# Performance work log

Hardware: AMD Instinct MI355X
Metric: run time of the kernel (lower is better)

The kernel has to match this reference:

```python
import jax, jax.numpy as jnp
import numpy as np

N_CLUSTERS = 64
N_GHOST = 2
EPS = 1e-12  # F.normalize eps


def setup_inputs() -> dict:
    key = jax.random.key(0)
    k1, k2, k3, k4 = jax.random.split(key, 4)
    n_utts, feat_dim, duration = 16, 256, 1500
    x = jax.random.normal(k1, (n_utts, feat_dim, duration), dtype=jnp.float32)
    centroids = jax.random.uniform(k2, (N_CLUSTERS, feat_dim), dtype=jnp.float32)
    # NetVLAD init ties linear.weight = 2*alpha*centroids(+ghosts); here independent params suffice for a math baseline
    lin_w = jax.random.normal(k3, (N_CLUSTERS + N_GHOST, feat_dim), dtype=jnp.float32)
    lin_b = jax.random.normal(k4, (N_CLUSTERS + N_GHOST,), dtype=jnp.float32)
    return {"x": x, "centroids": centroids, "lin_w": lin_w, "lin_b": lin_b}


def reference(x, centroids, lin_w, lin_b):
    # x: [u, f, t] -> [u, t, f]
    n_utts = x.shape[0]
    xt = jnp.transpose(x, (0, 2, 1))
    # soft assignments over clusters+ghosts, then drop ghost columns
    logits = jnp.einsum('utf,cf->utc', xt, lin_w) + lin_b  # [u,t,C+G]
    a = jax.nn.softmax(logits, axis=2)[..., :N_CLUSTERS]   # [u,t,C]
    # Fused NetVLAD aggregation (algebraically identical to
    # sum_t a[u,t,c] * (x[u,t,:] - centroids[c,:]) without materializing
    # the [u,t,C,f] residual tensor):
    comp = jnp.einsum('utc,utf->ucf', a, xt) - a.sum(axis=1)[..., None] * centroids  # [u,C,f]
    # intra-normalization (F.normalize p=2 over feat dim)
    comp = comp / jnp.maximum(jnp.linalg.norm(comp, axis=2, keepdims=True), EPS)
    sv = comp.reshape(n_utts, -1)  # [u, C*f]
    sv = sv / jnp.maximum(jnp.linalg.norm(sv, axis=1, keepdims=True), EPS)
    return sv
```

## Files before the change

### kernel.cpp

```cpp
#include <hip/hip_runtime.h>
#include <math.h>


#define NU 16
#define NF 256
#define NT 1500
#define NC 64
#define NCG 66
#define EPSN 1e-12f

#define T_CHUNK 96
#define N_CHUNKS 16

__device__ __forceinline__ float blk_reduce_sum(float v, float* sbuf) {
    #pragma unroll
    for (int off = 32; off > 0; off >>= 1) v += __shfl_down(v, off, 64);
    const int lane = threadIdx.x & 63, wv = threadIdx.x >> 6;
    if (lane == 0) sbuf[wv] = v;
    __syncthreads();
    float r = sbuf[0] + sbuf[1] + sbuf[2] + sbuf[3];
    __syncthreads();
    return r;
}

__global__ __launch_bounds__(256) void k1_assign(
        const float* __restrict__ x, const float* __restrict__ lin_w,
        const float* __restrict__ lin_b, float* __restrict__ a_ws) {
    const int u    = blockIdx.y;
    const int t0   = blockIdx.x * 64;
    const int tid  = threadIdx.x;
    const int lane = tid & 63;
    const int wave = tid >> 6;
    const int t    = t0 + lane;
    const int tc   = (t < NT) ? t : (NT - 1);

    __shared__ float wsm[4][NCG][16];
    __shared__ float red[2][NCG][64];

    float acc[NCG];
    #pragma unroll
    for (int c = 0; c < NCG; ++c) acc[c] = 0.0f;

    for (int fc = 0; fc < 4; ++fc) {
        const int fbase = wave * 64 + fc * 16;
        for (int idx = lane; idx < NCG * 16; idx += 64) {
            const int c = idx >> 4, k = idx & 15;
            wsm[wave][c][k] = lin_w[c * NF + fbase + k];
        }
        __syncthreads();

        float xv[16];
        #pragma unroll
        for (int k = 0; k < 16; ++k)
            xv[k] = x[(u * NF + fbase + k) * NT + tc];

        #pragma unroll
        for (int c = 0; c < NCG; ++c) {
            const float4* wr = (const float4*)(&wsm[wave][c][0]);
            const float4 w0 = wr[0], w1 = wr[1], w2 = wr[2], w3 = wr[3];
            acc[c] += w0.x*xv[0]  + w0.y*xv[1]  + w0.z*xv[2]  + w0.w*xv[3]
                    + w1.x*xv[4]  + w1.y*xv[5]  + w1.z*xv[6]  + w1.w*xv[7]
                    + w2.x*xv[8]  + w2.y*xv[9]  + w2.z*xv[10] + w2.w*xv[11]
                    + w3.x*xv[12] + w3.y*xv[13] + w3.z*xv[14] + w3.w*xv[15];
        }
        __syncthreads();
    }

    if (wave >= 2) {
        #pragma unroll
        for (int c = 0; c < NCG; ++c) red[wave - 2][c][lane] = acc[c];
    }
    __syncthreads();
    if (wave < 2) {
        #pragma unroll
        for (int c = 0; c < NCG; ++c) acc[c] += red[wave][c][lane];
    }
    __syncthreads();
    if (wave == 1) {
        #pragma unroll
        for (int c = 0; c < NCG; ++c) red[0][c][lane] = acc[c];
    }
    __syncthreads();
    if (wave == 0) {
        #pragma unroll
        for (int c = 0; c < NCG; ++c) acc[c] += red[0][c][lane] + lin_b[c];
        float m = -INFINITY;
        #pragma unroll
        for (int c = 0; c < NCG; ++c) m = fmaxf(m, acc[c]);
        float s = 0.0f;
        #pragma unroll
        for (int c = 0; c < NCG; ++c) { acc[c] = __expf(acc[c] - m); s += acc[c]; }
        const float inv = 1.0f / s;
        if (t < NT) {
            #pragma unroll
            for (int c = 0; c < NC; ++c)
                a_ws[(u * NC + c) * NT + t] = acc[c] * inv;
        }
    }
}

__global__ __launch_bounds__(256) void k2_agg(
        const float* __restrict__ x, const float* __restrict__ a_ws,
        float* __restrict__ partial) {
    const int u = blockIdx.y, chunk = blockIdx.x;
    const int tid = threadIdx.x;
    const int t0 = chunk * T_CHUNK;
    const int t_end = min(t0 + T_CHUNK, NT);

    __shared__ float Asm[64][17];
    __shared__ float Xsm[256][17];

    float acc[8][8];
    #pragma unroll
    for (int i = 0; i < 8; ++i)
        #pragma unroll
        for (int j = 0; j < 8; ++j) acc[i][j] = 0.0f;

    const int cs = tid >> 2;
    const int ks = (tid & 3) * 4;
    const int c_base = (tid >> 5) * 8;
    const int fl = tid & 31;

    for (int k0 = t0; k0 < t_end; k0 += 16) {
        const int rem = t_end - k0;
        {
            const float* rp = a_ws + (u * NC + cs) * NT + k0 + ks;
            float4 v;
            if (ks + 3 < rem) v = *(const float4*)rp;
            else {
                v.x = (ks + 0 < rem) ? rp[0] : 0.0f;
                v.y = (ks + 1 < rem) ? rp[1] : 0.0f;
                v.z = (ks + 2 < rem) ? rp[2] : 0.0f;
                v.w = (ks + 3 < rem) ? rp[3] : 0.0f;
            }
            Asm[cs][ks+0] = v.x; Asm[cs][ks+1] = v.y;
            Asm[cs][ks+2] = v.z; Asm[cs][ks+3] = v.w;
        }
        #pragma unroll
        for (int r = 0; r < 4; ++r) {
            const int f = cs + 64 * r;
            const float* rp = x + (u * NF + f) * NT + k0 + ks;
            float4 v;
            if (ks + 3 < rem) v = *(const float4*)rp;
            else {
                v.x = (ks + 0 < rem) ? rp[0] : 0.0f;
                v.y = (ks + 1 < rem) ? rp[1] : 0.0f;
                v.z = (ks + 2 < rem) ? rp[2] : 0.0f;
                v.w = (ks + 3 < rem) ? rp[3] : 0.0f;
            }
            Xsm[f][ks+0] = v.x; Xsm[f][ks+1] = v.y;
            Xsm[f][ks+2] = v.z; Xsm[f][ks+3] = v.w;
        }
        __syncthreads();

        #pragma unroll 4
        for (int k = 0; k < 16; ++k) {
            float av[8], xv[8];
            #pragma unroll
            for (int i = 0; i < 8; ++i) av[i] = Asm[c_base + i][k];
            #pragma unroll
            for (int j = 0; j < 8; ++j) xv[j] = Xsm[fl + 32 * j][k];
            #pragma unroll
            for (int i = 0; i < 8; ++i)
                #pragma unroll
                for (int j = 0; j < 8; ++j) acc[i][j] += av[i] * xv[j];
        }
        __syncthreads();
    }

    #pragma unroll
    for (int i = 0; i < 8; ++i) {
        const int c = c_base + i;
        float* op = partial + ((chunk * NU + u) * NC + c) * NF;
        #pragma unroll
        for (int j = 0; j < 8; ++j) op[fl + 32 * j] = acc[i][j];
    }
}

__global__ __launch_bounds__(256) void k3_norm(
        const float* __restrict__ a_ws, const float* __restrict__ partial,
        const float* __restrict__ centroids, float* __restrict__ compn,
        float* __restrict__ rowsq) {
    const int c = blockIdx.x, u = blockIdx.y;
    const int tid = threadIdx.x;
    __shared__ float sbuf[4];

    float s = 0.0f;
    const float* arow = a_ws + (u * NC + c) * NT;
    for (int i = tid; i < NT; i += 256) s += arow[i];
    const float asum = blk_reduce_sum(s, sbuf);

    float val = 0.0f;
    #pragma unroll
    for (int ch = 0; ch < N_CHUNKS; ++ch)
        val += partial[((ch * NU + u) * NC + c) * NF + tid];
    val -= asum * centroids[c * NF + tid];

    const float ss = blk_reduce_sum(val * val, sbuf);
    const float d  = fmaxf(sqrtf(ss), EPSN);
    compn[(u * NC + c) * NF + tid] = val / d;
    if (tid == 0) rowsq[u * NC + c] = ss / (d * d);
}

__global__ __launch_bounds__(256) void k4_scale(
        const float* __restrict__ compn, const float* __restrict__ rowsq,
        float* __restrict__ out) {
    const int u = blockIdx.y;
    const int tid = threadIdx.x;
    float gss = 0.0f;
    #pragma unroll
    for (int cc = 0; cc < NC; ++cc) gss += rowsq[u * NC + cc];
    const float inv = 1.0f / fmaxf(sqrtf(gss), EPSN);
    const int base = u * (NC * NF) + blockIdx.x * 4096;
    #pragma unroll
    for (int r = 0; r < 16; ++r) {
        const int idx = base + r * 256 + tid;
        out[idx] = compn[idx] * inv;
    }
}

extern "C" void kernel_launch(void* const* d_in, const int* in_sizes, int n_in,
                              void* d_out, int out_size, void* d_ws, size_t ws_size,
                              hipStream_t stream) {
    (void)in_sizes; (void)n_in; (void)out_size; (void)ws_size;
    const float* x         = (const float*)d_in[0];
    const float* centroids = (const float*)d_in[1];
    const float* lin_w     = (const float*)d_in[2];
    const float* lin_b     = (const float*)d_in[3];
    float* out = (float*)d_out;

    float* ws      = (float*)d_ws;
    float* a_ws    = ws;
    float* partial = a_ws + NU * NC * NT;
    float* compn   = partial + N_CHUNKS * NU * NC * NF;
    float* rowsq   = compn + NU * NC * NF;

    dim3 blk(256);
    hipLaunchKernelGGL(k1_assign, dim3(24, NU), blk, 0, stream, x, lin_w, lin_b, a_ws);
    hipLaunchKernelGGL(k2_agg,    dim3(N_CHUNKS, NU), blk, 0, stream, x, a_ws, partial);
    hipLaunchKernelGGL(k3_norm,   dim3(NC, NU), blk, 0, stream, a_ws, partial, centroids, compn, rowsq);
    hipLaunchKernelGGL(k4_scale,  dim3(4, NU), blk, 0, stream, compn, rowsq, out);
}
```

Before: 141.8 us.

## Use wave-uniform scalar weight loads in assign and restage aggregation over feature halves

The assign kernel drops LDS staging of lin_w and its block barriers. Each wave now reads weights directly through wave-uniform addresses, which can become scalar loads. The aggregation kernel stages a whole time chunk of x for half the features into LDS once. It reads assignment rows through wave-uniform float4 loads and splits the grid over feature halves to double the block count. The intent is to cut barrier and LDS traffic and raise occupancy, at the risk of more global/scalar cache pressure and less register blocking per thread.

```diff
diff --git a/kernel.cpp b/kernel.cpp
--- a/kernel.cpp
+++ b/kernel.cpp
@@ -30,40 +30,29 @@
     const int t0   = blockIdx.x * 64;
     const int tid  = threadIdx.x;
     const int lane = tid & 63;
-    const int wave = tid >> 6;
+    const int wave = __builtin_amdgcn_readfirstlane(tid >> 6);
     const int t    = t0 + lane;
     const int tc   = (t < NT) ? t : (NT - 1);
 
-    __shared__ float wsm[4][NCG][16];
     __shared__ float red[2][NCG][64];
 
     float acc[NCG];
     #pragma unroll
     for (int c = 0; c < NCG; ++c) acc[c] = 0.0f;
 
-    for (int fc = 0; fc < 4; ++fc) {
-        const int fbase = wave * 64 + fc * 16;
-        for (int idx = lane; idx < NCG * 16; idx += 64) {
-            const int c = idx >> 4, k = idx & 15;
-            wsm[wave][c][k] = lin_w[c * NF + fbase + k];
-        }
-        __syncthreads();
-
-        float xv[16];
-        #pragma unroll
-        for (int k = 0; k < 16; ++k)
-            xv[k] = x[(u * NF + fbase + k) * NT + tc];
-
+    const float* wbase = lin_w + wave * 64;
+    const float* xbase = x + (u * NF + wave * 64) * NT + tc;
+
+    #pragma unroll 2
+    for (int kq = 0; kq < 16; ++kq) {
+        float xv[4];
+        #pragma unroll
+        for (int q = 0; q < 4; ++q) xv[q] = xbase[(kq * 4 + q) * NT];
         #pragma unroll
         for (int c = 0; c < NCG; ++c) {
-            const float4* wr = (const float4*)(&wsm[wave][c][0]);
-            const float4 w0 = wr[0], w1 = wr[1], w2 = wr[2], w3 = wr[3];
-            acc[c] += w0.x*xv[0]  + w0.y*xv[1]  + w0.z*xv[2]  + w0.w*xv[3]
-                    + w1.x*xv[4]  + w1.y*xv[5]  + w1.z*xv[6]  + w1.w*xv[7]
-                    + w2.x*xv[8]  + w2.y*xv[9]  + w2.z*xv[10] + w2.w*xv[11]
-                    + w3.x*xv[12] + w3.y*xv[13] + w3.z*xv[14] + w3.w*xv[15];
-        }
-        __syncthreads();
+            const float4 w = *(const float4*)(wbase + c * NF + kq * 4);
+            acc[c] += w.x * xv[0] + w.y * xv[1] + w.z * xv[2] + w.w * xv[3];
+        }
     }
 
     if (wave >= 2) {
@@ -102,78 +91,67 @@
 __global__ __launch_bounds__(256) void k2_agg(
         const float* __restrict__ x, const float* __restrict__ a_ws,
         float* __restrict__ partial) {
-    const int u = blockIdx.y, chunk = blockIdx.x;
-    const int tid = threadIdx.x;
-    const int t0 = chunk * T_CHUNK;
-    const int t_end = min(t0 + T_CHUNK, NT);
-
-    __shared__ float Asm[64][17];
-    __shared__ float Xsm[256][17];
-
-    float acc[8][8];
-    #pragma unroll
-    for (int i = 0; i < 8; ++i)
-        #pragma unroll
-        for (int j = 0; j < 8; ++j) acc[i][j] = 0.0f;
-
-    const int cs = tid >> 2;
-    const int ks = (tid & 3) * 4;
-    const int c_base = (tid >> 5) * 8;
-    const int fl = tid & 31;
-
-    for (int k0 = t0; k0 < t_end; k0 += 16) {
-        const int rem = t_end - k0;
-        {
-            const float* rp = a_ws + (u * NC + cs) * NT + k0 + ks;
+    const int chunk = blockIdx.x;
+    const int fh    = blockIdx.y;
+    const int u     = blockIdx.z;
+    const int t0    = chunk * T_CHUNK;
+    const int nt    = min(T_CHUNK, NT - t0);
+    const int tid   = threadIdx.x;
+
+    __shared__ float Xsm[128][T_CHUNK + 4];
+
+    const int r0 = tid >> 2, l4 = tid & 3;
+    #pragma unroll
+    for (int g = 0; g < 2; ++g) {
+        const int fr = r0 + 64 * g;
+        const float* rp = x + (u * NF + fh * 128 + fr) * NT + t0;
+        #pragma unroll
+        for (int s = 0; s < 6; ++s) {
+            const int col = (l4 + 4 * s) * 4;
             float4 v;
-            if (ks + 3 < rem) v = *(const float4*)rp;
+            if (col + 4 <= nt) v = *(const float4*)(rp + col);
             else {
-                v.x = (ks + 0 < rem) ? rp[0] : 0.0f;
-                v.y = (ks + 1 < rem) ? rp[1] : 0.0f;
-                v.z = (ks + 2 < rem) ? rp[2] : 0.0f;
-                v.w = (ks + 3 < rem) ? rp[3] : 0.0f;
+                v.x = (col + 0 < nt) ? rp[col + 0] : 0.0f;
+                v.y = (col + 1 < nt) ? rp[col + 1] : 0.0f;
+                v.z = (col + 2 < nt) ? rp[col + 2] : 0.0f;
+                v.w = (col + 3 < nt) ? rp[col + 3] : 0.0f;
             }
-            Asm[cs][ks+0] = v.x; Asm[cs][ks+1] = v.y;
-            Asm[cs][ks+2] = v.z; Asm[cs][ks+3] = v.w;
-        }
-        #pragma unroll
-        for (int r = 0; r < 4; ++r) {
-            const int f = cs + 64 * r;
-            const float* rp = x + (u * NF + f) * NT + k0 + ks;
-            float4 v;
-            if (ks + 3 < rem) v = *(const float4*)rp;
-            else {
-                v.x = (ks + 0 < rem) ? rp[0] : 0.0f;
-                v.y = (ks + 1 < rem) ? rp[1] : 0.0f;
-                v.z = (ks + 2 < rem) ? rp[2] : 0.0f;
-                v.w = (ks + 3 < rem) ? rp[3] : 0.0f;
-            }
-            Xsm[f][ks+0] = v.x; Xsm[f][ks+1] = v.y;
-            Xsm[f][ks+2] = v.z; Xsm[f][ks+3] = v.w;
-        }
-        __syncthreads();
-
-        #pragma unroll 4
-        for (int k = 0; k < 16; ++k) {
-            float av[8], xv[8];
+            *(float4*)&Xsm[fr][col] = v;
+        }
+    }
+    __syncthreads();
+
+    const int wv = __builtin_amdgcn_readfirstlane(tid >> 6);
+    const int c0 = wv * 16;
+    const int fl = tid & 63;
+
+    float acc[16][2];
+    #pragma unroll
+    for (int i = 0; i < 16; ++i) { acc[i][0] = 0.0f; acc[i][1] = 0.0f; }
+
+    const float* abase = a_ws + (u * NC + c0) * NT + t0;
+    const int kq_end = nt >> 2;
+
+    for (int kq = 0; kq < kq_end; ++kq) {
+        float4 xv[2];
+        #pragma unroll
+        for (int j = 0; j < 2; ++j)
+            xv[j] = *(const float4*)&Xsm[fl + 64 * j][kq * 4];
+        #pragma unroll
+        for (int i = 0; i < 16; ++i) {
+            const float4 a4 = *(const float4*)(abase + i * NT + kq * 4);
             #pragma unroll
-            for (int i = 0; i < 8; ++i) av[i] = Asm[c_base + i][k];
-            #pragma unroll
-            for (int j = 0; j < 8; ++j) xv[j] = Xsm[fl + 32 * j][k];
-            #pragma unroll
-            for (int i = 0; i < 8; ++i)
-                #pragma unroll
-                for (int j = 0; j < 8; ++j) acc[i][j] += av[i] * xv[j];
-        }
-        __syncthreads();
-    }
-
-    #pragma unroll
-    for (int i = 0; i < 8; ++i) {
-        const int c = c_base + i;
-        float* op = partial + ((chunk * NU + u) * NC + c) * NF;
-        #pragma unroll
-        for (int j = 0; j < 8; ++j) op[fl + 32 * j] = acc[i][j];
+            for (int j = 0; j < 2; ++j)
+                acc[i][j] += a4.x * xv[j].x + a4.y * xv[j].y
+                           + a4.z * xv[j].z + a4.w * xv[j].w;
+        }
+    }
+
+    #pragma unroll
+    for (int i = 0; i < 16; ++i) {
+        float* op = partial + ((chunk * NU + u) * NC + c0 + i) * NF + fh * 128;
+        op[fl]      = acc[i][0];
+        op[fl + 64] = acc[i][1];
     }
 }
 
@@ -237,7 +215,7 @@
 
     dim3 blk(256);
     hipLaunchKernelGGL(k1_assign, dim3(24, NU), blk, 0, stream, x, lin_w, lin_b, a_ws);
-    hipLaunchKernelGGL(k2_agg,    dim3(N_CHUNKS, NU), blk, 0, stream, x, a_ws, partial);
+    hipLaunchKernelGGL(k2_agg,    dim3(N_CHUNKS, 2, NU), blk, 0, stream, x, a_ws, partial);
     hipLaunchKernelGGL(k3_norm,   dim3(NC, NU), blk, 0, stream, a_ws, partial, centroids, compn, rowsq);
     hipLaunchKernelGGL(k4_scale,  dim3(4, NU), blk, 0, stream, compn, rowsq, out);
 }
```

Result: slower. 172.5 us (+21.6%).
